# Performance work log

Measured on AMD Instinct MI355X. Metric: run time of the kernel, lower is better.

The kernel has to match this reference:

```python
import jax, jax.numpy as jnp
import numpy as np

D = 1024
N_HEADS = 16


def build_masks(H, W):
    # Row-major grid: token i -> (i // W, i % W). True = attend.
    idx = jnp.arange(H * W)
    r, c = idx // W, idx % W
    ri, rj = r[:, None], r[None, :]
    ci, cj = c[:, None], c[None, :]
    lr = (ri > rj) | ((ri == rj) & (ci >= cj))
    rl = (ri < rj) | ((ri == rj) & (ci <= cj))
    td = (ci > cj) | ((ci == cj) & (ri >= rj))
    bu = (ci < cj) | ((ci == cj) & (ri <= rj))
    return lr, rl, td, bu


def dir_attn(x, w_qkv, w_o, mask):
    # x: (B,T,D); w_qkv: (3D,D); w_o: (D,D); mask: (T,T) bool
    B, T, Dm = x.shape
    hd = Dm // N_HEADS
    qkv = (x @ w_qkv.T).reshape(B, T, 3, N_HEADS, hd)
    q = qkv[:, :, 0].transpose(0, 2, 1, 3)  # (B,H,T,hd)
    k = qkv[:, :, 1].transpose(0, 2, 1, 3)
    v = qkv[:, :, 2].transpose(0, 2, 1, 3)
    scores = jnp.einsum('bhqd,bhkd->bhqk', q, k) / np.sqrt(hd)
    scores = jnp.where(mask[None, None], scores, -jnp.inf)
    attn = jax.nn.softmax(scores, axis=-1)
    y = jnp.einsum('bhqk,bhkd->bhqd', attn, v)
    y = y.transpose(0, 2, 1, 3).reshape(B, T, Dm)
    return y @ w_o.T


def rmsnorm(x, w, eps=1e-6):
    norm = jax.lax.rsqrt(jnp.mean(jnp.square(x.astype(jnp.float32)), axis=-1, keepdims=True) + eps)
    return (x.astype(jnp.float32) * norm).astype(x.dtype) * w


def setup_inputs() -> dict:
    key = jax.random.key(0)
    ks = jax.random.split(key, 13)
    s = 0.02
    inp = {
        'x': jax.random.normal(ks[0], (4, 1024, D), dtype=jnp.float32),
        'w_qkv_lr': jax.random.normal(ks[1], (3 * D, D), dtype=jnp.float32) * s,
        'w_o_lr':   jax.random.normal(ks[2], (D, D), dtype=jnp.float32) * s,
        'w_qkv_rl': jax.random.normal(ks[3], (3 * D, D), dtype=jnp.float32) * s,
        'w_o_rl':   jax.random.normal(ks[4], (D, D), dtype=jnp.float32) * s,
        'w_qkv_td': jax.random.normal(ks[5], (3 * D, D), dtype=jnp.float32) * s,
        'w_o_td':   jax.random.normal(ks[6], (D, D), dtype=jnp.float32) * s,
        'w_qkv_bu': jax.random.normal(ks[7], (3 * D, D), dtype=jnp.float32) * s,
        'w_o_bu':   jax.random.normal(ks[8], (D, D), dtype=jnp.float32) * s,
        'w_gate':   jax.random.normal(ks[9], (4 * D, 4 * D), dtype=jnp.float32) * s,
        'b_gate':   jnp.zeros((4 * D,), dtype=jnp.float32),
        'w_out':    jax.random.normal(ks[10], (D, 4 * D), dtype=jnp.float32) * s,
        'norm_w':   jnp.ones((D,), dtype=jnp.float32),
        'grid_h': 32,
        'grid_w': 32,
    }
    return inp


def reference(x, w_qkv_lr, w_o_lr, w_qkv_rl, w_o_rl, w_qkv_td, w_o_td,
              w_qkv_bu, w_o_bu, w_gate, b_gate, w_out, norm_w, grid_h, grid_w):
    m_lr, m_rl, m_td, m_bu = build_masks(grid_h, grid_w)
    h_lr = dir_attn(x, w_qkv_lr, w_o_lr, m_lr)
    h_rl = dir_attn(x, w_qkv_rl, w_o_rl, m_rl)
    h_td = dir_attn(x, w_qkv_td, w_o_td, m_td)
    h_bu = dir_attn(x, w_qkv_bu, w_o_bu, m_bu)
    concat = jnp.concatenate([h_lr, h_rl, h_td, h_bu], axis=-1)  # (B,T,4D)
    gate = jax.nn.sigmoid(concat @ w_gate.T + b_gate)
    fused = (gate * concat) @ w_out.T
    return rmsnorm(fused + x, norm_w)
```

## Files before the change

### kernel.cpp

```cpp
#include <hip/hip_runtime.h>
#include <hip/hip_bf16.h>
#include <math.h>


typedef __bf16 bf16_t;
typedef __bf16 bf16x4 __attribute__((ext_vector_type(4)));
typedef __bf16 bf16x8 __attribute__((ext_vector_type(8)));
typedef float  f32x4  __attribute__((ext_vector_type(4)));

#define MFMA16(a, b, c) __builtin_amdgcn_mfma_f32_16x16x32_bf16((a), (b), (c), 0, 0, 0)

__device__ __forceinline__ void async16(const bf16_t* g, bf16_t* l) {
  __builtin_amdgcn_global_load_lds((const __attribute__((address_space(1))) void*)g,
                                   (__attribute__((address_space(3))) void*)l,
                                   16, 0, 0);
}

__device__ __forceinline__ float dpp_max16(float x) {
  float t;
  t = __builtin_bit_cast(float, __builtin_amdgcn_update_dpp(0, __builtin_bit_cast(int, x), 0xB1, 0xF, 0xF, true));
  x = fmaxf(x, t);
  t = __builtin_bit_cast(float, __builtin_amdgcn_update_dpp(0, __builtin_bit_cast(int, x), 0x4E, 0xF, 0xF, true));
  x = fmaxf(x, t);
  t = __builtin_bit_cast(float, __builtin_amdgcn_update_dpp(0, __builtin_bit_cast(int, x), 0x124, 0xF, 0xF, true));
  x = fmaxf(x, t);
  t = __builtin_bit_cast(float, __builtin_amdgcn_update_dpp(0, __builtin_bit_cast(int, x), 0x128, 0xF, 0xF, true));
  x = fmaxf(x, t);
  return x;
}
__device__ __forceinline__ float dpp_sum16(float x) {
  float t;
  t = __builtin_bit_cast(float, __builtin_amdgcn_update_dpp(0, __builtin_bit_cast(int, x), 0xB1, 0xF, 0xF, true));
  x += t;
  t = __builtin_bit_cast(float, __builtin_amdgcn_update_dpp(0, __builtin_bit_cast(int, x), 0x4E, 0xF, 0xF, true));
  x += t;
  t = __builtin_bit_cast(float, __builtin_amdgcn_update_dpp(0, __builtin_bit_cast(int, x), 0x124, 0xF, 0xF, true));
  x += t;
  t = __builtin_bit_cast(float, __builtin_amdgcn_update_dpp(0, __builtin_bit_cast(int, x), 0x128, 0xF, 0xF, true));
  x += t;
  return x;
}

struct Ptr4 { const bf16_t* p[4]; };

__device__ __forceinline__ int perm_t(int p, int dir) {
  int q = (dir & 1) ? (1023 - p) : p;
  if (dir >= 2) q = ((q & 31) << 5) | (q >> 5);
  return q;
}

struct CvtDesc {
  const float* src[9];
  bf16_t* dst[9];
  int n8[9];
};

__device__ __forceinline__ void cvt8(const float* in, bf16_t* out, int i) {
  const float4 a = ((const float4*)in)[i * 2];
  const float4 b = ((const float4*)in)[i * 2 + 1];
  bf16x8 o;
  o[0] = (bf16_t)a.x; o[1] = (bf16_t)a.y; o[2] = (bf16_t)a.z; o[3] = (bf16_t)a.w;
  o[4] = (bf16_t)b.x; o[5] = (bf16_t)b.y; o[6] = (bf16_t)b.z; o[7] = (bf16_t)b.w;
  ((bf16x8*)out)[i] = o;
}

__global__ __launch_bounds__(256) void cvt9_k(CvtDesc d) {
  const int seg = blockIdx.y;
  const int i = blockIdx.x * 256 + threadIdx.x;
  if (i >= d.n8[seg]) return;
  cvt8(d.src[seg], d.dst[seg], i);
}

template <int MODE>
__global__ __launch_bounds__(512, 2) void gemm_bt2(
    const bf16_t* __restrict__ A, long sAz, int lda,
    Ptr4 B4, int ldb,
    void* __restrict__ Cv, long sCz, int ldc, int K, int koff,
    const float* __restrict__ bias,
    const bf16_t* __restrict__ gin,
    bf16_t* __restrict__ vtp, long sVz, int dirbase) {
  constexpr int BM = 256, BN = 256, BK = 64;
  (void)BM; (void)BN;
  __shared__ __align__(16) char smem[131072];

  const int z = blockIdx.z;
  const bf16_t* Ap = A + (long)z * sAz;
  const bf16_t* Bp = B4.p[z];
  const int tid = threadIdx.x;
  const int lane = tid & 63;
  const int wave = tid >> 6;
  const int l15 = lane & 15, qd = lane >> 4;
  const int wm = wave >> 2, wn = wave & 3;
  const int bm = blockIdx.y * 256, bn = blockIdx.x * 256;
  const int kz = (MODE == 3) ? z * koff : 0;
  const int NT = K / BK;

  const int row0 = tid >> 3;
  const int blkp = ((tid & 7) ^ (row0 & 7)) * 8;
  const bf16_t* gA = Ap + (long)(bm + row0) * lda + blkp + kz;
  const bf16_t* gB = Bp + (long)(bn + row0) * ldb + blkp + kz;
  char* const sm = (char*)smem;
  const int ldsT = tid * 16;

  const int xorv = (l15 & 7) << 4;
  const int aBase = (wm * 128 + l15) * 128;
  const int bBase = 32768 + (wn * 64 + l15) * 128;
  const int colk0 = (qd * 16) ^ xorv;
  const int colk1 = (64 + qd * 16) ^ xorv;

  f32x4 acc[8][4];
#pragma unroll
  for (int i = 0; i < 8; i++)
#pragma unroll
    for (int j = 0; j < 4; j++) acc[i][j] = (f32x4){0.f, 0.f, 0.f, 0.f};

#pragma unroll
  for (int u = 0; u < 4; u++)
    async16(gA + (long)(u * 64) * lda, (bf16_t*)(sm + u * 8192 + ldsT));
#pragma unroll
  for (int u = 0; u < 4; u++)
    async16(gB + (long)(u * 64) * ldb, (bf16_t*)(sm + 32768 + u * 8192 + ldsT));
  asm volatile("s_waitcnt vmcnt(0)" ::: "memory");
  __builtin_amdgcn_s_barrier();

  for (int kt = 0; kt < NT; ++kt) {
    const int c = kt & 1;
    const char* sa = sm + c * 65536;
    const int nb = (c ^ 1) * 65536;
    const long ko = (long)(kt + 1) * BK;
    bf16x8 bF[4][2];
#pragma unroll
    for (int p = 0; p < 4; ++p) {
      if (p == 0) {
#pragma unroll
        for (int n = 0; n < 4; ++n) {
          bF[n][0] = *(const bf16x8*)(sa + bBase + n * 2048 + colk0);
          bF[n][1] = *(const bf16x8*)(sa + bBase + n * 2048 + colk1);
        }
      }
      bf16x8 aF[2][2];
#pragma unroll
      for (int mm = 0; mm < 2; ++mm) {
        aF[mm][0] = *(const bf16x8*)(sa + aBase + (p * 2 + mm) * 2048 + colk0);
        aF[mm][1] = *(const bf16x8*)(sa + aBase + (p * 2 + mm) * 2048 + colk1);
      }
      if (kt + 1 < NT) {
        if (p == 0) {
#pragma unroll
          for (int u = 0; u < 4; u++)
            async16(gA + (long)(u * 64) * lda + ko,
                    (bf16_t*)(sm + nb + u * 8192 + ldsT));
        } else if (p == 1) {
#pragma unroll
          for (int u = 0; u < 4; u++)
            async16(gB + (long)(u * 64) * ldb + ko,
                    (bf16_t*)(sm + nb + 32768 + u * 8192 + ldsT));
        }
      }
      __builtin_amdgcn_s_barrier();
      asm volatile("s_waitcnt lgkmcnt(0)" ::: "memory");
      __builtin_amdgcn_s_setprio(1);
#pragma unroll
      for (int kh = 0; kh < 2; ++kh)
#pragma unroll
        for (int mm = 0; mm < 2; ++mm)
#pragma unroll
          for (int n = 0; n < 4; ++n)
            acc[p * 2 + mm][n] =
                MFMA16(aF[mm][kh], bF[n][kh], acc[p * 2 + mm][n]);
      __builtin_amdgcn_s_setprio(0);
      __builtin_amdgcn_s_barrier();
    }
    if (kt + 1 < NT) {
      asm volatile("s_waitcnt vmcnt(0)" ::: "memory");
      __builtin_amdgcn_s_barrier();
    }
  }

  if constexpr (MODE == 4) {
    const int dir = dirbase + z;
    if (bn < 2048) {
      bf16_t* qkz = (bf16_t*)Cv + (long)z * sCz;
      float* sC = (float*)smem;
#pragma unroll
      for (int p = 0; p < 4; ++p) {
        if (p) __syncthreads();
        if (wm == (p >> 1)) {
#pragma unroll
          for (int mm = 0; mm < 4; ++mm) {
            const int m = (p & 1) * 4 + mm;
#pragma unroll
            for (int n = 0; n < 4; ++n)
#pragma unroll
              for (int r = 0; r < 4; ++r)
                sC[(mm * 16 + qd * 4 + r) * 260 + wn * 64 + n * 16 + l15] =
                    acc[m][n][r];
          }
        }
        __syncthreads();
#pragma unroll
        for (int i = 0; i < 8; ++i) {
          const int idx = i * 512 + tid;
          const int rl = idx >> 6, c4 = (idx & 63) * 4;
          const float4 v4 = *(const float4*)&sC[rl * 260 + c4];
          const int grow = bm + p * 64 + rl;
          const int prow = (grow & ~1023) | perm_t(grow & 1023, dir);
          bf16x4 o;
          o[0] = (bf16_t)v4.x; o[1] = (bf16_t)v4.y;
          o[2] = (bf16_t)v4.z; o[3] = (bf16_t)v4.w;
          *(bf16x4*)(qkz + (long)prow * ldc + bn + c4) = o;
        }
      }
    } else {
      bf16_t* vz = vtp + (long)z * sVz;
      float* sCt = (float*)smem;
#pragma unroll
      for (int p = 0; p < 4; ++p) {
        if (p) __syncthreads();
        if (wm == (p >> 1)) {
#pragma unroll
          for (int mm = 0; mm < 4; ++mm) {
            const int m = (p & 1) * 4 + mm;
#pragma unroll
            for (int n = 0; n < 4; ++n)
#pragma unroll
              for (int r = 0; r < 4; ++r)
                sCt[(wn * 64 + n * 16 + l15) * 68 + mm * 16 + qd * 4 + r] =
                    acc[m][n][r];
          }
        }
        __syncthreads();
#pragma unroll
        for (int i = 0; i < 8; ++i) {
          const int idx = i * 512 + tid;
          const int col = idx >> 4, tq = idx & 15;
          const float4 v4 = *(const float4*)&sCt[col * 68 + tq * 4];
          const int t0 = (bm & 1023) + p * 64 + tq * 4;
          const int bb = bm >> 10;
          const int ch = bn + col - 2048;
          bf16_t* vrow =
              vz + (((long)bb * 16 + (ch >> 6)) * 64 + (ch & 63)) * 1024;
          if (dir == 0) {
            bf16x4 o;
            o[0] = (bf16_t)v4.x; o[1] = (bf16_t)v4.y;
            o[2] = (bf16_t)v4.z; o[3] = (bf16_t)v4.w;
            *(bf16x4*)(vrow + t0) = o;
          } else if (dir == 1) {
            bf16x4 o;
            o[0] = (bf16_t)v4.w; o[1] = (bf16_t)v4.z;
            o[2] = (bf16_t)v4.y; o[3] = (bf16_t)v4.x;
            *(bf16x4*)(vrow + (1020 - t0)) = o;
          } else {
            vrow[perm_t(t0 + 0, dir)] = (bf16_t)v4.x;
            vrow[perm_t(t0 + 1, dir)] = (bf16_t)v4.y;
            vrow[perm_t(t0 + 2, dir)] = (bf16_t)v4.z;
            vrow[perm_t(t0 + 3, dir)] = (bf16_t)v4.w;
          }
        }
      }
    }
  } else {
    float* sC = (float*)smem;
#pragma unroll
    for (int p = 0; p < 4; ++p) {
      if (p) __syncthreads();
      if (wm == (p >> 1)) {
#pragma unroll
        for (int mm = 0; mm < 4; ++mm) {
          const int m = (p & 1) * 4 + mm;
#pragma unroll
          for (int n = 0; n < 4; ++n)
#pragma unroll
            for (int r = 0; r < 4; ++r)
              sC[(mm * 16 + qd * 4 + r) * 260 + wn * 64 + n * 16 + l15] =
                  acc[m][n][r];
        }
      }
      __syncthreads();
#pragma unroll
      for (int i = 0; i < 8; ++i) {
        const int idx = i * 512 + tid;
        const int rl = idx >> 6, c4 = (idx & 63) * 4;
        const float4 v4 = *(const float4*)&sC[rl * 260 + c4];
        const int grow = bm + p * 64 + rl;
        const int gcol = bn + c4;
        const long goff = (long)grow * ldc + gcol;
        if constexpr (MODE == 0) {
          bf16x4 o;
          o[0] = (bf16_t)v4.x; o[1] = (bf16_t)v4.y;
          o[2] = (bf16_t)v4.z; o[3] = (bf16_t)v4.w;
          *(bf16x4*)((bf16_t*)Cv + (long)z * sCz + goff) = o;
        } else if constexpr (MODE == 1) {
          const float4 bb = *(const float4*)&bias[gcol];
          const bf16x4 gv = *(const bf16x4*)&gin[goff];
          bf16x4 o;
          o[0] = (bf16_t)((float)gv[0] / (1.f + __expf(-(v4.x + bb.x))));
          o[1] = (bf16_t)((float)gv[1] / (1.f + __expf(-(v4.y + bb.y))));
          o[2] = (bf16_t)((float)gv[2] / (1.f + __expf(-(v4.z + bb.z))));
          o[3] = (bf16_t)((float)gv[3] / (1.f + __expf(-(v4.w + bb.w))));
          *(bf16x4*)((bf16_t*)Cv + goff) = o;
        } else {
          *(float4*)((float*)Cv + (long)z * sCz + goff) = v4;
        }
      }
    }
  }
}

template <int MODE>
__global__ __launch_bounds__(256) void gemm_bt(
    const bf16_t* __restrict__ A, long sAz, int lda,
    Ptr4 B4, int ldb,
    void* __restrict__ Cv, long sCz, int ldc, int K, int koff,
    const float* __restrict__ bias,
    const bf16_t* __restrict__ gin,
    bf16_t* __restrict__ vtp, long sVz, int dirbase) {
  constexpr int BM = 128, BN = 128, BK = 32;
  __shared__ __align__(16) char smem[18432];
  bf16_t* sA = (bf16_t*)smem;
  bf16_t* sB = (bf16_t*)(smem + BM * BK * 2);
  float* sC = (float*)smem;

  const int z = blockIdx.z;
  const bf16_t* Ap = A + (long)z * sAz;
  const bf16_t* Bp = B4.p[z];
  const int tid = threadIdx.x;
  const int wave = tid >> 6, lane = tid & 63;
  const int lane15 = lane & 15, quad = lane >> 4;
  const int bm = blockIdx.y * BM, bn = blockIdx.x * BN;
  const int wm = (wave >> 1) * 64, wn = (wave & 1) * 64;

  f32x4 acc[4][4];
#pragma unroll
  for (int i = 0; i < 4; i++)
#pragma unroll
    for (int j = 0; j < 4; j++) acc[i][j] = (f32x4){0.f, 0.f, 0.f, 0.f};

  const int srow = wave * 16 + (lane >> 2);
  const int skoff = (lane & 3) * 8;
  const int kz = (MODE == 3) ? z * koff : 0;
  const bf16_t* ga = Ap + (long)(bm + srow) * lda + skoff + kz;
  const bf16_t* gb = Bp + (long)(bn + srow) * ldb + skoff + kz;
  bf16_t* la = &sA[srow * BK + skoff];
  bf16_t* lb = &sB[srow * BK + skoff];

  for (int k0 = 0; k0 < K; k0 += BK) {
    __syncthreads();
    async16(ga + k0, la);
    async16(ga + k0 + (long)64 * lda, la + 64 * BK);
    async16(gb + k0, lb);
    async16(gb + k0 + (long)64 * ldb, lb + 64 * BK);
    __syncthreads();

    bf16x8 af[4], bfv[4];
#pragma unroll
    for (int i = 0; i < 4; i++)
      af[i] = *(const bf16x8*)&sA[(wm + i * 16 + lane15) * BK + quad * 8];
#pragma unroll
    for (int j = 0; j < 4; j++)
      bfv[j] = *(const bf16x8*)&sB[(wn + j * 16 + lane15) * BK + quad * 8];
#pragma unroll
    for (int i = 0; i < 4; i++)
#pragma unroll
      for (int j = 0; j < 4; j++)
        acc[i][j] = MFMA16(af[i], bfv[j], acc[i][j]);
  }

  __syncthreads();

  if constexpr (MODE == 4) {
    const int dir = dirbase + z;
    if (bn < 2048) {
      bf16_t* qkz = (bf16_t*)Cv + (long)z * sCz;
#pragma unroll
      for (int p = 0; p < 4; p++) {
        if (p) __syncthreads();
        const int sr = (wm >> 2) + quad * 4;
#pragma unroll
        for (int r = 0; r < 4; r++)
#pragma unroll
          for (int j = 0; j < 4; j++)
            sC[(sr + r) * 144 + wn + j * 16 + lane15] = acc[p][j][r];
        __syncthreads();
#pragma unroll
        for (int c = 0; c < 4; c++) {
          const int idx = c * 256 + tid;
          const int srr = idx >> 5, chunk = idx & 31;
          const float4 v4 = *(const float4*)&sC[srr * 144 + chunk * 4];
          const int grow = bm + p * 16 + (srr & 15) + (srr >> 4) * 64;
          const int prow = (grow & ~1023) | perm_t(grow & 1023, dir);
          bf16x4 o;
          o[0] = (bf16_t)v4.x; o[1] = (bf16_t)v4.y;
          o[2] = (bf16_t)v4.z; o[3] = (bf16_t)v4.w;
          *(bf16x4*)(qkz + (long)prow * 2048 + bn + chunk * 4) = o;
        }
      }
    } else {
      bf16_t* vz = vtp + (long)z * sVz;
      float* sCt = sC;
#pragma unroll
      for (int p = 0; p < 2; p++)
#pragma unroll
        for (int q = 0; q < 2; q++) {
          if (p || q) __syncthreads();
          if ((wave & 1) == q) {
#pragma unroll
            for (int ii = 0; ii < 2; ii++) {
              const int i = 2 * p + ii;
              const int srb = (wm >> 1) + ii * 16 + quad * 4;
#pragma unroll
              for (int r = 0; r < 4; r++)
#pragma unroll
                for (int j = 0; j < 4; j++)
                  sCt[(j * 16 + lane15) * 68 + srb + r] = acc[i][j][r];
            }
          }
          __syncthreads();
#pragma unroll
          for (int c = 0; c < 4; c++) {
            const int idx = c * 256 + tid;
            const int col = idx >> 4, tq = idx & 15;
            const int srr0 = (tq & 7) * 4 + (tq >> 3) * 32;
            const float4 v4 = *(const float4*)&sCt[col * 68 + srr0];
            const int t0 = (bm & 1023) + p * 32 + (srr0 & 31) + (srr0 >> 5) * 64;
            const int bb = bm >> 10;
            const int ch = bn + 64 * q + col - 2048;
            bf16_t* vrow =
                vz + (((long)bb * 16 + (ch >> 6)) * 64 + (ch & 63)) * 1024;
            if (dir == 0) {
              bf16x4 o;
              o[0] = (bf16_t)v4.x; o[1] = (bf16_t)v4.y;
              o[2] = (bf16_t)v4.z; o[3] = (bf16_t)v4.w;
              *(bf16x4*)(vrow + t0) = o;
            } else if (dir == 1) {
              bf16x4 o;
              o[0] = (bf16_t)v4.w; o[1] = (bf16_t)v4.z;
              o[2] = (bf16_t)v4.y; o[3] = (bf16_t)v4.x;
              *(bf16x4*)(vrow + (1020 - t0)) = o;
            } else {
              vrow[perm_t(t0 + 0, dir)] = (bf16_t)v4.x;
              vrow[perm_t(t0 + 1, dir)] = (bf16_t)v4.y;
              vrow[perm_t(t0 + 2, dir)] = (bf16_t)v4.z;
              vrow[perm_t(t0 + 3, dir)] = (bf16_t)v4.w;
            }
          }
        }
    }
  } else {
#pragma unroll
    for (int p = 0; p < 4; p++) {
      if (p) __syncthreads();
      const int sr = (wm >> 2) + quad * 4;
#pragma unroll
      for (int r = 0; r < 4; r++)
#pragma unroll
        for (int j = 0; j < 4; j++)
          sC[(sr + r) * 144 + wn + j * 16 + lane15] = acc[p][j][r];
      __syncthreads();
#pragma unroll
      for (int c = 0; c < 4; c++) {
        const int idx = c * 256 + tid;
        const int srr = idx >> 5, chunk = idx & 31;
        const float4 v4 = *(const float4*)&sC[srr * 144 + chunk * 4];
        const int grow = bm + p * 16 + (srr & 15) + (srr >> 4) * 64;
        const int gcol = bn + chunk * 4;
        const long goff = (long)grow * ldc + gcol;
        if constexpr (MODE == 0) {
          bf16x4 o;
          o[0] = (bf16_t)v4.x; o[1] = (bf16_t)v4.y;
          o[2] = (bf16_t)v4.z; o[3] = (bf16_t)v4.w;
          *(bf16x4*)((bf16_t*)Cv + (long)z * sCz + goff) = o;
        } else if constexpr (MODE == 1) {
          const float4 bb = *(const float4*)&bias[gcol];
          const bf16x4 gv = *(const bf16x4*)&gin[goff];
          bf16x4 o;
          o[0] = (bf16_t)((float)gv[0] / (1.f + __expf(-(v4.x + bb.x))));
          o[1] = (bf16_t)((float)gv[1] / (1.f + __expf(-(v4.y + bb.y))));
          o[2] = (bf16_t)((float)gv[2] / (1.f + __expf(-(v4.z + bb.z))));
          o[3] = (bf16_t)((float)gv[3] / (1.f + __expf(-(v4.w + bb.w))));
          *(bf16x4*)((bf16_t*)Cv + goff) = o;
        } else {
          *(float4*)((float*)Cv + (long)z * sCz + goff) = v4;
        }
      }
    }
  }
}

__global__ __launch_bounds__(256, 3) void attn_k(
    const bf16_t* __restrict__ qk, long sQz,
    const bf16_t* __restrict__ vt, long sVz,
    bf16_t* __restrict__ y, long sYz, int dir0) {
  const int zi = blockIdx.y >> 6;
  const int bh = blockIdx.y & 63;
  const int dir = dir0 + zi;
  const int b = bh >> 4, h = bh & 15;
  const int qt = (int)(gridDim.x - 1 - blockIdx.x);
  const int tid = threadIdx.x;
  const int wave = tid >> 6, lane = tid & 63;
  const int lane15 = lane & 15, quad = lane >> 4;
  const int hoff = h * 64;
  const bf16_t* base = qk + (long)zi * sQz + (long)b * 1024 * 2048;
  const bf16_t* vth = vt + (long)zi * sVz + ((long)b * 16 + h) * 64 * 1024;
  bf16_t* yd = y + (long)zi * sYz;

  __shared__ __align__(16) bf16_t sK[64 * 72];
  __shared__ __align__(16) bf16_t sVt[64 * 72];
  __shared__ __align__(16) bf16_t sP[4][32 * 72];

  bf16x8 qa[2][2];
#pragma unroll
  for (int g = 0; g < 2; g++) {
    const int row = qt * 128 + wave * 32 + g * 16 + lane15;
    qa[g][0] = *(const bf16x8*)(base + (long)row * 2048 + hoff + quad * 8);
    qa[g][1] = *(const bf16x8*)(base + (long)row * 2048 + hoff + 32 + quad * 8);
  }

  const float FNEG = -1e30f;
  float mrow[2][4], lrow[2][4];
  f32x4 o[2][4];
#pragma unroll
  for (int g = 0; g < 2; g++)
#pragma unroll
    for (int r = 0; r < 4; r++) { mrow[g][r] = FNEG; lrow[g][r] = 0.f; }
#pragma unroll
  for (int g = 0; g < 2; g++)
#pragma unroll
    for (int d4 = 0; d4 < 4; d4++) o[g][d4] = (f32x4){0.f, 0.f, 0.f, 0.f};

  const int krow = tid >> 3, kd = (tid & 7) * 8;
  const int vd = tid >> 2, pc = (tid & 3) * 8;
  const bf16_t* kb_g = base + 1024 + hoff;

  bf16x8 kA = *(const bf16x8*)(kb_g + (long)krow * 2048 + kd);
  bf16x8 kB = *(const bf16x8*)(kb_g + (long)(32 + krow) * 2048 + kd);
  bf16x8 vA = *(const bf16x8*)(vth + (long)vd * 1024 + pc);
  bf16x8 vB = *(const bf16x8*)(vth + (long)vd * 1024 + 32 + pc);

  const int ktiles = 2 * qt + 2;
  for (int kt = 0; kt < ktiles; kt++) {
    __syncthreads();
    *(bf16x8*)&sK[krow * 72 + kd] = kA;
    *(bf16x8*)&sK[(krow + 32) * 72 + kd] = kB;
    *(bf16x8*)&sVt[vd * 72 + pc] = vA;
    *(bf16x8*)&sVt[vd * 72 + 32 + pc] = vB;
    __syncthreads();
    if (kt + 1 < ktiles) {
      const int nb = (kt + 1) * 64;
      kA = *(const bf16x8*)(kb_g + (long)(nb + krow) * 2048 + kd);
      kB = *(const bf16x8*)(kb_g + (long)(nb + 32 + krow) * 2048 + kd);
      vA = *(const bf16x8*)(vth + (long)vd * 1024 + nb + pc);
      vB = *(const bf16x8*)(vth + (long)vd * 1024 + nb + 32 + pc);
    }
    const int kbase = kt * 64;

    bf16x8 kb[4][2];
#pragma unroll
    for (int ns = 0; ns < 4; ns++) {
      kb[ns][0] = *(const bf16x8*)&sK[(ns * 16 + lane15) * 72 + quad * 8];
      kb[ns][1] = *(const bf16x8*)&sK[(ns * 16 + lane15) * 72 + 32 + quad * 8];
    }
    f32x4 s[2][4];
#pragma unroll
    for (int g = 0; g < 2; g++)
#pragma unroll
      for (int ns = 0; ns < 4; ns++) {
        f32x4 t = (f32x4){0.f, 0.f, 0.f, 0.f};
        t = MFMA16(qa[g][0], kb[ns][0], t);
        t = MFMA16(qa[g][1], kb[ns][1], t);
        s[g][ns] = t;
      }
#pragma unroll
    for (int g = 0; g < 2; g++) {
      const int qc = qt * 128 + wave * 32 + g * 16 + quad * 4;
#pragma unroll
      for (int ns = 0; ns < 4; ns++) {
        const int kp = kbase + ns * 16 + lane15;
#pragma unroll
        for (int r = 0; r < 4; r++) {
          const float v = s[g][ns][r] * 0.125f;
          s[g][ns][r] = (kp <= qc + r) ? v : FNEG;
        }
      }
    }
#pragma unroll
    for (int g = 0; g < 2; g++) {
      float alpha[4];
#pragma unroll
      for (int r = 0; r < 4; r++) {
        float tm = fmaxf(fmaxf(s[g][0][r], s[g][1][r]),
                         fmaxf(s[g][2][r], s[g][3][r]));
        tm = dpp_max16(tm);
        const float mn = fmaxf(mrow[g][r], tm);
        alpha[r] = __expf(mrow[g][r] - mn);
        mrow[g][r] = mn;
      }
#pragma unroll
      for (int ns = 0; ns < 4; ns++)
#pragma unroll
        for (int r = 0; r < 4; r++)
          s[g][ns][r] = __expf(s[g][ns][r] - mrow[g][r]);
#pragma unroll
      for (int r = 0; r < 4; r++) {
        float ts = (s[g][0][r] + s[g][1][r]) + (s[g][2][r] + s[g][3][r]);
        ts = dpp_sum16(ts);
        lrow[g][r] = lrow[g][r] * alpha[r] + ts;
      }
#pragma unroll
      for (int d4 = 0; d4 < 4; d4++)
#pragma unroll
        for (int r = 0; r < 4; r++) o[g][d4][r] *= alpha[r];
#pragma unroll
      for (int ns = 0; ns < 4; ns++)
#pragma unroll
        for (int r = 0; r < 4; r++)
          sP[wave][(g * 16 + quad * 4 + r) * 72 + ns * 16 + lane15] =
              (bf16_t)s[g][ns][r];
    }
    bf16x8 vb[4][2];
#pragma unroll
    for (int d4 = 0; d4 < 4; d4++) {
      vb[d4][0] = *(const bf16x8*)&sVt[(d4 * 16 + lane15) * 72 + quad * 8];
      vb[d4][1] = *(const bf16x8*)&sVt[(d4 * 16 + lane15) * 72 + 32 + quad * 8];
    }
#pragma unroll
    for (int g = 0; g < 2; g++) {
      const bf16x8 pa0 = *(const bf16x8*)&sP[wave][(g * 16 + lane15) * 72 + quad * 8];
      const bf16x8 pa1 = *(const bf16x8*)&sP[wave][(g * 16 + lane15) * 72 + 32 + quad * 8];
#pragma unroll
      for (int d4 = 0; d4 < 4; d4++) {
        o[g][d4] = MFMA16(pa0, vb[d4][0], o[g][d4]);
        o[g][d4] = MFMA16(pa1, vb[d4][1], o[g][d4]);
      }
    }
  }

#pragma unroll
  for (int g = 0; g < 2; g++)
#pragma unroll
    for (int r = 0; r < 4; r++) {
      const float rinv = 1.f / fmaxf(lrow[g][r], 1e-20f);
#pragma unroll
      for (int d4 = 0; d4 < 4; d4++)
        sP[wave][(g * 16 + quad * 4 + r) * 72 + d4 * 16 + lane15] =
            (bf16_t)(o[g][d4][r] * rinv);
    }
#pragma unroll
  for (int g = 0; g < 2; g++) {
    const bf16x8 o0 = *(const bf16x8*)&sP[wave][(g * 16 + lane15) * 72 + quad * 16];
    const bf16x8 o1 = *(const bf16x8*)&sP[wave][(g * 16 + lane15) * 72 + quad * 16 + 8];
    const int tok = perm_t(qt * 128 + wave * 32 + g * 16 + lane15, dir);
    bf16_t* yr = yd + ((long)b * 1024 + tok) * 1024 + hoff + quad * 16;
    *(bf16x8*)yr = o0;
    *(bf16x8*)(yr + 8) = o1;
  }
}

__global__ __launch_bounds__(256) void rmsnorm_k(const float* __restrict__ p0,
                                                 const float* __restrict__ p1,
                                                 const float* __restrict__ p2,
                                                 const float* __restrict__ p3,
                                                 const float* __restrict__ x,
                                                 const float* __restrict__ w,
                                                 float* __restrict__ out) {
  const int row = blockIdx.x, tid = threadIdx.x;
  const long off = (long)row * 1024;
  const float4 a = ((const float4*)(p0 + off))[tid];
  const float4 bq = ((const float4*)(p1 + off))[tid];
  const float4 c = ((const float4*)(x + off))[tid];
  float4 v;
  v.x = a.x + bq.x + c.x;
  v.y = a.y + bq.y + c.y;
  v.z = a.z + bq.z + c.z;
  v.w = a.w + bq.w + c.w;
  if (p2) {
    const float4 d = ((const float4*)(p2 + off))[tid];
    const float4 e = ((const float4*)(p3 + off))[tid];
    v.x += d.x + e.x;
    v.y += d.y + e.y;
    v.z += d.z + e.z;
    v.w += d.w + e.w;
  }
  float ss = v.x * v.x + v.y * v.y + v.z * v.z + v.w * v.w;
#pragma unroll
  for (int o2 = 32; o2 >= 1; o2 >>= 1) ss += __shfl_xor(ss, o2);
  __shared__ float wsum[4];
  if ((tid & 63) == 0) wsum[tid >> 6] = ss;
  __syncthreads();
  const float tot = wsum[0] + wsum[1] + wsum[2] + wsum[3];
  const float norm = rsqrtf(tot * (1.f / 1024.f) + 1e-6f);
  const float4 wv = ((const float4*)w)[tid];
  v.x = v.x * norm * wv.x;
  v.y = v.y * norm * wv.y;
  v.z = v.z * norm * wv.z;
  v.w = v.w * norm * wv.w;
  ((float4*)(out + off))[tid] = v;
}

extern "C" void kernel_launch(void* const* d_in, const int* in_sizes, int n_in,
                              void* d_out, int out_size, void* d_ws, size_t ws_size,
                              hipStream_t stream) {
  (void)in_sizes; (void)n_in; (void)out_size;
  const float* xf = (const float*)d_in[0];
  const float* wqkv_f[4] = {(const float*)d_in[1], (const float*)d_in[3],
                            (const float*)d_in[5], (const float*)d_in[7]};
  const float* wo_f[4] = {(const float*)d_in[2], (const float*)d_in[4],
                          (const float*)d_in[6], (const float*)d_in[8]};
  const float* wgate_f = (const float*)d_in[9];
  const float* bgate_f = (const float*)d_in[10];
  const float* wout_f = (const float*)d_in[11];
  const float* normw_f = (const float*)d_in[12];

  const long MB = 1l << 20;
  char* ws = (char*)d_ws;
  const dim3 blk(256);
  const dim3 blk2(512);
  const bool batched = ws_size >= (size_t)(168 * MB);
  const long sQK = 4096l * 2048;
  const long sVT = 4096l * 1024;
  const long sY  = 4096l * 1024;

  if (batched) {
    bf16_t* x_c    = (bf16_t*)(ws);
    bf16_t* wq_c   = (bf16_t*)(ws + 8 * MB);
    bf16_t* wo_c   = (bf16_t*)(ws + 32 * MB);
    bf16_t* qk     = (bf16_t*)(ws + 40 * MB);
    bf16_t* vt     = (bf16_t*)(ws + 104 * MB);
    bf16_t* y      = (bf16_t*)(ws + 136 * MB);
    bf16_t* concat = (bf16_t*)(ws + 40 * MB);
    bf16_t* wg_c   = (bf16_t*)(ws + 72 * MB);
    bf16_t* wout_c = (bf16_t*)(ws);
    float*  part4  = (float*)(ws + 40 * MB);
    bf16_t* gated  = y;

    {
      CvtDesc cd;
      cd.src[0] = xf; cd.dst[0] = x_c; cd.n8[0] = 4194304 / 8;
      for (int d = 0; d < 4; d++) {
        cd.src[1 + d] = wqkv_f[d];
        cd.dst[1 + d] = wq_c + (long)d * 3145728;
        cd.n8[1 + d] = 3145728 / 8;
        cd.src[5 + d] = wo_f[d];
        cd.dst[5 + d] = wo_c + (long)d * 1048576;
        cd.n8[5 + d] = 1048576 / 8;
      }
      cvt9_k<<<dim3(2048, 9), blk, 0, stream>>>(cd);
    }
    {
      Ptr4 bq{{wq_c, wq_c + 3145728, wq_c + 2l * 3145728, wq_c + 3l * 3145728}};
      gemm_bt2<4><<<dim3(12, 16, 4), blk2, 0, stream>>>(
          x_c, 0, 1024, bq, 1024, qk, sQK, 2048, 1024, 0, nullptr, nullptr,
          vt, sVT, 0);
    }
    attn_k<<<dim3(8, 256), blk, 0, stream>>>(qk, sQK, vt, sVT, y, sY, 0);
    {
      CvtDesc cd;
      for (int s = 0; s < 9; s++) cd.n8[s] = 0;
      cd.src[0] = wgate_f; cd.dst[0] = wg_c; cd.n8[0] = 16777216 / 8;
      cd.src[1] = wout_f; cd.dst[1] = wout_c; cd.n8[1] = 4194304 / 8;
      cvt9_k<<<dim3(8192, 2), blk, 0, stream>>>(cd);
    }
    {
      Ptr4 b4{{wo_c, wo_c + 1048576, wo_c + 2097152, wo_c + 3145728}};
      gemm_bt2<0><<<dim3(4, 16, 4), blk2, 0, stream>>>(
          y, sY, 1024, b4, 1024, concat, 1024, 4096, 1024, 0, nullptr, nullptr,
          nullptr, 0, 0);
    }
    {
      Ptr4 b4{{wg_c, wg_c, wg_c, wg_c}};
      gemm_bt2<1><<<dim3(16, 16, 1), blk2, 0, stream>>>(
          concat, 0, 4096, b4, 4096, gated, 0, 4096, 4096, 0, bgate_f, concat,
          nullptr, 0, 0);
    }
    {
      Ptr4 b4{{wout_c, wout_c, wout_c, wout_c}};
      gemm_bt2<3><<<dim3(4, 16, 4), blk2, 0, stream>>>(
          gated, 0, 4096, b4, 4096, part4, (long)4096 * 1024, 1024, 1024, 1024,
          nullptr, nullptr, nullptr, 0, 0);
    }
    rmsnorm_k<<<dim3(4096), blk, 0, stream>>>(
        part4, part4 + (long)4096 * 1024, part4 + 2l * 4096 * 1024,
        part4 + 3l * 4096 * 1024, xf, normw_f, (float*)d_out);
  } else {
    bf16_t* x_c    = (bf16_t*)(ws);
    bf16_t* wq_c   = (bf16_t*)(ws + 8 * MB);
    bf16_t* qk_d   = (bf16_t*)(ws + 32 * MB);
    bf16_t* vt_d   = (bf16_t*)(ws + 48 * MB);
    bf16_t* wo_c   = (bf16_t*)(ws + 56 * MB);
    bf16_t* y      = (bf16_t*)(ws + 64 * MB);
    bf16_t* concat = (bf16_t*)(ws);
    bf16_t* wg_c   = (bf16_t*)(ws + 32 * MB);
    bf16_t* wout_c = (bf16_t*)(ws);
    float*  part   = (float*)(ws + 8 * MB);
    bf16_t* gated  = y;

    {
      CvtDesc cd;
      cd.src[0] = xf; cd.dst[0] = x_c; cd.n8[0] = 4194304 / 8;
      for (int d = 0; d < 4; d++) {
        cd.src[1 + d] = wqkv_f[d];
        cd.dst[1 + d] = wq_c + (long)d * 3145728;
        cd.n8[1 + d] = 3145728 / 8;
        cd.src[5 + d] = wo_f[d];
        cd.dst[5 + d] = wo_c + (long)d * 1048576;
        cd.n8[5 + d] = 1048576 / 8;
      }
      cvt9_k<<<dim3(2048, 9), blk, 0, stream>>>(cd);
    }
    for (int d = 0; d < 4; d++) {
      const bf16_t* wq_d = wq_c + (long)d * 3145728;
      Ptr4 bq{{wq_d, wq_d, wq_d, wq_d}};
      gemm_bt<4><<<dim3(24, 32, 1), blk, 0, stream>>>(
          x_c, 0, 1024, bq, 1024, qk_d, 0, 2048, 1024, 0, nullptr, nullptr,
          vt_d, 0, d);
      attn_k<<<dim3(8, 64), blk, 0, stream>>>(qk_d, 0, vt_d, 0,
                                              y + (long)d * sY, 0, d);
    }
    {
      Ptr4 b4{{wo_c, wo_c + 1048576, wo_c + 2097152, wo_c + 3145728}};
      gemm_bt<0><<<dim3(8, 32, 4), blk, 0, stream>>>(
          y, sY, 1024, b4, 1024, concat, 1024, 4096, 1024, 0, nullptr, nullptr,
          nullptr, 0, 0);
    }
    {
      CvtDesc cd;
      for (int s = 0; s < 9; s++) cd.n8[s] = 0;
      cd.src[0] = wgate_f; cd.dst[0] = wg_c; cd.n8[0] = 16777216 / 8;
      cvt9_k<<<dim3(8192, 1), blk, 0, stream>>>(cd);
    }
    {
      Ptr4 b4{{wg_c, wg_c, wg_c, wg_c}};
      gemm_bt<1><<<dim3(32, 32, 1), blk, 0, stream>>>(
          concat, 0, 4096, b4, 4096, gated, 0, 4096, 4096, 0, bgate_f, concat,
          nullptr, 0, 0);
    }
    {
      CvtDesc cd;
      for (int s = 0; s < 9; s++) cd.n8[s] = 0;
      cd.src[0] = wout_f; cd.dst[0] = wout_c; cd.n8[0] = 4194304 / 8;
      cvt9_k<<<dim3(2048, 1), blk, 0, stream>>>(cd);
    }
    {
      Ptr4 b4{{wout_c, wout_c, wout_c, wout_c}};
      gemm_bt<3><<<dim3(8, 32, 2), blk, 0, stream>>>(
          gated, 0, 4096, b4, 4096, part, (long)4096 * 1024, 1024, 2048, 2048,
          nullptr, nullptr, nullptr, 0, 0);
    }
    rmsnorm_k<<<dim3(4096), blk, 0, stream>>>(part, part + (long)4096 * 1024,
                                              nullptr, nullptr,
                                              xf, normw_f, (float*)d_out);
  }
}
```

Measured before the change: 697.2 us.

## Pair causal query tiles per attention block and fold softmax scale into K

Each attention block now handles two query tiles, a long one and a short one (7-bx and bx), so causal work is balanced across blocks. Block indices are remapped with a swizzle, likely to improve L2 locality. The 1/sqrt(hd) scale moves into the K epilogue of the QKV GEMM, so the attention loop no longer multiplies every score. Masking runs only on diagonal tiles, and the O/l rescale is skipped when no row max changes. The GEMM mainloop drops one barrier per k-step by merging the vmcnt wait into the last sub-step. Launch bounds are raised to 4 waves per SIMD, which may increase register pressure or cause spills.

```diff
diff --git a/kernel.cpp b/kernel.cpp
--- a/kernel.cpp
+++ b/kernel.cpp
@@ -169,10 +169,8 @@
             acc[p * 2 + mm][n] =
                 MFMA16(aF[mm][kh], bF[n][kh], acc[p * 2 + mm][n]);
       __builtin_amdgcn_s_setprio(0);
-      __builtin_amdgcn_s_barrier();
-    }
-    if (kt + 1 < NT) {
-      asm volatile("s_waitcnt vmcnt(0)" ::: "memory");
+      if (p == 3 && kt + 1 < NT)
+        asm volatile("s_waitcnt vmcnt(0)" ::: "memory");
       __builtin_amdgcn_s_barrier();
     }
   }
@@ -181,6 +179,7 @@
     const int dir = dirbase + z;
     if (bn < 2048) {
       bf16_t* qkz = (bf16_t*)Cv + (long)z * sCz;
+      const float ksc = (bn >= 1024) ? 0.125f : 1.0f;
       float* sC = (float*)smem;
 #pragma unroll
       for (int p = 0; p < 4; ++p) {
@@ -206,8 +205,8 @@
           const int grow = bm + p * 64 + rl;
           const int prow = (grow & ~1023) | perm_t(grow & 1023, dir);
           bf16x4 o;
-          o[0] = (bf16_t)v4.x; o[1] = (bf16_t)v4.y;
-          o[2] = (bf16_t)v4.z; o[3] = (bf16_t)v4.w;
+          o[0] = (bf16_t)(v4.x * ksc); o[1] = (bf16_t)(v4.y * ksc);
+          o[2] = (bf16_t)(v4.z * ksc); o[3] = (bf16_t)(v4.w * ksc);
           *(bf16x4*)(qkz + (long)prow * ldc + bn + c4) = o;
         }
       }
@@ -372,6 +371,7 @@
     const int dir = dirbase + z;
     if (bn < 2048) {
       bf16_t* qkz = (bf16_t*)Cv + (long)z * sCz;
+      const float ksc = (bn >= 1024) ? 0.125f : 1.0f;
 #pragma unroll
       for (int p = 0; p < 4; p++) {
         if (p) __syncthreads();
@@ -390,8 +390,8 @@
           const int grow = bm + p * 16 + (srr & 15) + (srr >> 4) * 64;
           const int prow = (grow & ~1023) | perm_t(grow & 1023, dir);
           bf16x4 o;
-          o[0] = (bf16_t)v4.x; o[1] = (bf16_t)v4.y;
-          o[2] = (bf16_t)v4.z; o[3] = (bf16_t)v4.w;
+          o[0] = (bf16_t)(v4.x * ksc); o[1] = (bf16_t)(v4.y * ksc);
+          o[2] = (bf16_t)(v4.z * ksc); o[3] = (bf16_t)(v4.w * ksc);
           *(bf16x4*)(qkz + (long)prow * 2048 + bn + chunk * 4) = o;
         }
       }
@@ -487,15 +487,18 @@
   }
 }
 
-__global__ __launch_bounds__(256, 3) void attn_k(
+__global__ __launch_bounds__(256, 4) void attn_k(
     const bf16_t* __restrict__ qk, long sQz,
     const bf16_t* __restrict__ vt, long sVz,
     bf16_t* __restrict__ y, long sYz, int dir0) {
-  const int zi = blockIdx.y >> 6;
-  const int bh = blockIdx.y & 63;
+  const int p0 = blockIdx.y * 4 + blockIdx.x;
+  const int chunk = gridDim.y >> 1;
+  const int lg = (p0 & 7) * chunk + (p0 >> 3);
+  const int bx = lg & 3, by = lg >> 2;
+  const int zi = by >> 6;
+  const int bh = by & 63;
   const int dir = dir0 + zi;
   const int b = bh >> 4, h = bh & 15;
-  const int qt = (int)(gridDim.x - 1 - blockIdx.x);
   const int tid = threadIdx.x;
   const int wave = tid >> 6, lane = tid & 63;
   const int lane15 = lane & 15, quad = lane >> 4;
@@ -508,151 +511,173 @@
   __shared__ __align__(16) bf16_t sVt[64 * 72];
   __shared__ __align__(16) bf16_t sP[4][32 * 72];
 
-  bf16x8 qa[2][2];
-#pragma unroll
-  for (int g = 0; g < 2; g++) {
-    const int row = qt * 128 + wave * 32 + g * 16 + lane15;
-    qa[g][0] = *(const bf16x8*)(base + (long)row * 2048 + hoff + quad * 8);
-    qa[g][1] = *(const bf16x8*)(base + (long)row * 2048 + hoff + 32 + quad * 8);
-  }
-
-  const float FNEG = -1e30f;
-  float mrow[2][4], lrow[2][4];
-  f32x4 o[2][4];
-#pragma unroll
-  for (int g = 0; g < 2; g++)
-#pragma unroll
-    for (int r = 0; r < 4; r++) { mrow[g][r] = FNEG; lrow[g][r] = 0.f; }
-#pragma unroll
-  for (int g = 0; g < 2; g++)
-#pragma unroll
-    for (int d4 = 0; d4 < 4; d4++) o[g][d4] = (f32x4){0.f, 0.f, 0.f, 0.f};
-
   const int krow = tid >> 3, kd = (tid & 7) * 8;
   const int vd = tid >> 2, pc = (tid & 3) * 8;
   const bf16_t* kb_g = base + 1024 + hoff;
-
-  bf16x8 kA = *(const bf16x8*)(kb_g + (long)krow * 2048 + kd);
-  bf16x8 kB = *(const bf16x8*)(kb_g + (long)(32 + krow) * 2048 + kd);
-  bf16x8 vA = *(const bf16x8*)(vth + (long)vd * 1024 + pc);
-  bf16x8 vB = *(const bf16x8*)(vth + (long)vd * 1024 + 32 + pc);
-
-  const int ktiles = 2 * qt + 2;
-  for (int kt = 0; kt < ktiles; kt++) {
-    __syncthreads();
-    *(bf16x8*)&sK[krow * 72 + kd] = kA;
-    *(bf16x8*)&sK[(krow + 32) * 72 + kd] = kB;
-    *(bf16x8*)&sVt[vd * 72 + pc] = vA;
-    *(bf16x8*)&sVt[vd * 72 + 32 + pc] = vB;
-    __syncthreads();
-    if (kt + 1 < ktiles) {
-      const int nb = (kt + 1) * 64;
-      kA = *(const bf16x8*)(kb_g + (long)(nb + krow) * 2048 + kd);
-      kB = *(const bf16x8*)(kb_g + (long)(nb + 32 + krow) * 2048 + kd);
-      vA = *(const bf16x8*)(vth + (long)vd * 1024 + nb + pc);
-      vB = *(const bf16x8*)(vth + (long)vd * 1024 + nb + 32 + pc);
-    }
-    const int kbase = kt * 64;
-
-    bf16x8 kb[4][2];
-#pragma unroll
-    for (int ns = 0; ns < 4; ns++) {
-      kb[ns][0] = *(const bf16x8*)&sK[(ns * 16 + lane15) * 72 + quad * 8];
-      kb[ns][1] = *(const bf16x8*)&sK[(ns * 16 + lane15) * 72 + 32 + quad * 8];
-    }
-    f32x4 s[2][4];
+  const float FNEG = -1e30f;
+
+  for (int pass = 0; pass < 2; ++pass) {
+    const int qt = pass ? bx : 7 - bx;
+
+    bf16x8 qa[2][2];
+#pragma unroll
+    for (int g = 0; g < 2; g++) {
+      const int row = qt * 128 + wave * 32 + g * 16 + lane15;
+      qa[g][0] = *(const bf16x8*)(base + (long)row * 2048 + hoff + quad * 8);
+      qa[g][1] = *(const bf16x8*)(base + (long)row * 2048 + hoff + 32 + quad * 8);
+    }
+
+    float mrow[2][4], lrow[2][4];
+    f32x4 o[2][4];
 #pragma unroll
     for (int g = 0; g < 2; g++)
 #pragma unroll
+      for (int r = 0; r < 4; r++) { mrow[g][r] = FNEG; lrow[g][r] = 0.f; }
+#pragma unroll
+    for (int g = 0; g < 2; g++)
+#pragma unroll
+      for (int d4 = 0; d4 < 4; d4++) o[g][d4] = (f32x4){0.f, 0.f, 0.f, 0.f};
+
+    bf16x8 kA = *(const bf16x8*)(kb_g + (long)krow * 2048 + kd);
+    bf16x8 kB = *(const bf16x8*)(kb_g + (long)(32 + krow) * 2048 + kd);
+    bf16x8 vA = *(const bf16x8*)(vth + (long)vd * 1024 + pc);
+    bf16x8 vB = *(const bf16x8*)(vth + (long)vd * 1024 + 32 + pc);
+
+    const int qlo = qt * 128 + wave * 32;
+    const int ktiles = 2 * qt + 2;
+    for (int kt = 0; kt < ktiles; kt++) {
+      __syncthreads();
+      *(bf16x8*)&sK[krow * 72 + kd] = kA;
+      *(bf16x8*)&sK[(krow + 32) * 72 + kd] = kB;
+      *(bf16x8*)&sVt[vd * 72 + pc] = vA;
+      *(bf16x8*)&sVt[vd * 72 + 32 + pc] = vB;
+      __syncthreads();
+      if (kt + 1 < ktiles) {
+        const int nb = (kt + 1) * 64;
+        kA = *(const bf16x8*)(kb_g + (long)(nb + krow) * 2048 + kd);
+        kB = *(const bf16x8*)(kb_g + (long)(nb + 32 + krow) * 2048 + kd);
+        vA = *(const bf16x8*)(vth + (long)vd * 1024 + nb + pc);
+        vB = *(const bf16x8*)(vth + (long)vd * 1024 + nb + 32 + pc);
+      }
+      const int kbase = kt * 64;
+
+      bf16x8 kb[4][2];
+#pragma unroll
       for (int ns = 0; ns < 4; ns++) {
-        f32x4 t = (f32x4){0.f, 0.f, 0.f, 0.f};
-        t = MFMA16(qa[g][0], kb[ns][0], t);
-        t = MFMA16(qa[g][1], kb[ns][1], t);
-        s[g][ns] = t;
+        kb[ns][0] = *(const bf16x8*)&sK[(ns * 16 + lane15) * 72 + quad * 8];
+        kb[ns][1] = *(const bf16x8*)&sK[(ns * 16 + lane15) * 72 + 32 + quad * 8];
+      }
+      f32x4 s[2][4];
+#pragma unroll
+      for (int g = 0; g < 2; g++)
+#pragma unroll
+        for (int ns = 0; ns < 4; ns++) {
+          f32x4 t = (f32x4){0.f, 0.f, 0.f, 0.f};
+          t = MFMA16(qa[g][0], kb[ns][0], t);
+          t = MFMA16(qa[g][1], kb[ns][1], t);
+          s[g][ns] = t;
+        }
+      if (kbase + 63 > qlo) {
+#pragma unroll
+        for (int g = 0; g < 2; g++) {
+          const int qc = qlo + g * 16 + quad * 4;
+#pragma unroll
+          for (int ns = 0; ns < 4; ns++) {
+            const int kp = kbase + ns * 16 + lane15;
+#pragma unroll
+            for (int r = 0; r < 4; r++)
+              if (kp > qc + r) s[g][ns][r] = FNEG;
+          }
+        }
+      }
+      float tm[2][4];
+#pragma unroll
+      for (int g = 0; g < 2; g++)
+#pragma unroll
+        for (int r = 0; r < 4; r++) {
+          float t = fmaxf(fmaxf(s[g][0][r], s[g][1][r]),
+                          fmaxf(s[g][2][r], s[g][3][r]));
+          tm[g][r] = dpp_max16(t);
+        }
+      bool up = false;
+#pragma unroll
+      for (int g = 0; g < 2; g++)
+#pragma unroll
+        for (int r = 0; r < 4; r++) up = up || (tm[g][r] > mrow[g][r]);
+      if (__any(up)) {
+#pragma unroll
+        for (int g = 0; g < 2; g++) {
+          float alpha[4];
+#pragma unroll
+          for (int r = 0; r < 4; r++) {
+            const float mn = fmaxf(mrow[g][r], tm[g][r]);
+            alpha[r] = __expf(mrow[g][r] - mn);
+            mrow[g][r] = mn;
+          }
+#pragma unroll
+          for (int r = 0; r < 4; r++) lrow[g][r] *= alpha[r];
+#pragma unroll
+          for (int d4 = 0; d4 < 4; d4++)
+#pragma unroll
+            for (int r = 0; r < 4; r++) o[g][d4][r] *= alpha[r];
+        }
+      }
+#pragma unroll
+      for (int g = 0; g < 2; g++) {
+#pragma unroll
+        for (int ns = 0; ns < 4; ns++)
+#pragma unroll
+          for (int r = 0; r < 4; r++)
+            s[g][ns][r] = __expf(s[g][ns][r] - mrow[g][r]);
+#pragma unroll
+        for (int r = 0; r < 4; r++) {
+          float ts = (s[g][0][r] + s[g][1][r]) + (s[g][2][r] + s[g][3][r]);
+          lrow[g][r] += dpp_sum16(ts);
+        }
+#pragma unroll
+        for (int ns = 0; ns < 4; ns++)
+#pragma unroll
+          for (int r = 0; r < 4; r++)
+            sP[wave][(g * 16 + quad * 4 + r) * 72 + ns * 16 + lane15] =
+                (bf16_t)s[g][ns][r];
+      }
+      bf16x8 vb[4][2];
+#pragma unroll
+      for (int d4 = 0; d4 < 4; d4++) {
+        vb[d4][0] = *(const bf16x8*)&sVt[(d4 * 16 + lane15) * 72 + quad * 8];
+        vb[d4][1] = *(const bf16x8*)&sVt[(d4 * 16 + lane15) * 72 + 32 + quad * 8];
+      }
+#pragma unroll
+      for (int g = 0; g < 2; g++) {
+        const bf16x8 pa0 = *(const bf16x8*)&sP[wave][(g * 16 + lane15) * 72 + quad * 8];
+        const bf16x8 pa1 = *(const bf16x8*)&sP[wave][(g * 16 + lane15) * 72 + 32 + quad * 8];
+#pragma unroll
+        for (int d4 = 0; d4 < 4; d4++) {
+          o[g][d4] = MFMA16(pa0, vb[d4][0], o[g][d4]);
+          o[g][d4] = MFMA16(pa1, vb[d4][1], o[g][d4]);
+        }
+      }
+    }
+
+#pragma unroll
+    for (int g = 0; g < 2; g++)
+#pragma unroll
+      for (int r = 0; r < 4; r++) {
+        const float rinv = 1.f / fmaxf(lrow[g][r], 1e-20f);
+#pragma unroll
+        for (int d4 = 0; d4 < 4; d4++)
+          sP[wave][(g * 16 + quad * 4 + r) * 72 + d4 * 16 + lane15] =
+              (bf16_t)(o[g][d4][r] * rinv);
       }
 #pragma unroll
     for (int g = 0; g < 2; g++) {
-      const int qc = qt * 128 + wave * 32 + g * 16 + quad * 4;
-#pragma unroll
-      for (int ns = 0; ns < 4; ns++) {
-        const int kp = kbase + ns * 16 + lane15;
-#pragma unroll
-        for (int r = 0; r < 4; r++) {
-          const float v = s[g][ns][r] * 0.125f;
-          s[g][ns][r] = (kp <= qc + r) ? v : FNEG;
-        }
-      }
-    }
-#pragma unroll
-    for (int g = 0; g < 2; g++) {
-      float alpha[4];
-#pragma unroll
-      for (int r = 0; r < 4; r++) {
-        float tm = fmaxf(fmaxf(s[g][0][r], s[g][1][r]),
-                         fmaxf(s[g][2][r], s[g][3][r]));
-        tm = dpp_max16(tm);
-        const float mn = fmaxf(mrow[g][r], tm);
-        alpha[r] = __expf(mrow[g][r] - mn);
-        mrow[g][r] = mn;
-      }
-#pragma unroll
-      for (int ns = 0; ns < 4; ns++)
-#pragma unroll
-        for (int r = 0; r < 4; r++)
-          s[g][ns][r] = __expf(s[g][ns][r] - mrow[g][r]);
-#pragma unroll
-      for (int r = 0; r < 4; r++) {
-        float ts = (s[g][0][r] + s[g][1][r]) + (s[g][2][r] + s[g][3][r]);
-        ts = dpp_sum16(ts);
-        lrow[g][r] = lrow[g][r] * alpha[r] + ts;
-      }
-#pragma unroll
-      for (int d4 = 0; d4 < 4; d4++)
-#pragma unroll
-        for (int r = 0; r < 4; r++) o[g][d4][r] *= alpha[r];
-#pragma unroll
-      for (int ns = 0; ns < 4; ns++)
-#pragma unroll
-        for (int r = 0; r < 4; r++)
-          sP[wave][(g * 16 + quad * 4 + r) * 72 + ns * 16 + lane15] =
-              (bf16_t)s[g][ns][r];
-    }
-    bf16x8 vb[4][2];
-#pragma unroll
-    for (int d4 = 0; d4 < 4; d4++) {
-      vb[d4][0] = *(const bf16x8*)&sVt[(d4 * 16 + lane15) * 72 + quad * 8];
-      vb[d4][1] = *(const bf16x8*)&sVt[(d4 * 16 + lane15) * 72 + 32 + quad * 8];
-    }
-#pragma unroll
-    for (int g = 0; g < 2; g++) {
-      const bf16x8 pa0 = *(const bf16x8*)&sP[wave][(g * 16 + lane15) * 72 + quad * 8];
-      const bf16x8 pa1 = *(const bf16x8*)&sP[wave][(g * 16 + lane15) * 72 + 32 + quad * 8];
-#pragma unroll
-      for (int d4 = 0; d4 < 4; d4++) {
-        o[g][d4] = MFMA16(pa0, vb[d4][0], o[g][d4]);
-        o[g][d4] = MFMA16(pa1, vb[d4][1], o[g][d4]);
-      }
-    }
-  }
-
-#pragma unroll
-  for (int g = 0; g < 2; g++)
-#pragma unroll
-    for (int r = 0; r < 4; r++) {
-      const float rinv = 1.f / fmaxf(lrow[g][r], 1e-20f);
-#pragma unroll
-      for (int d4 = 0; d4 < 4; d4++)
-        sP[wave][(g * 16 + quad * 4 + r) * 72 + d4 * 16 + lane15] =
-            (bf16_t)(o[g][d4][r] * rinv);
-    }
-#pragma unroll
-  for (int g = 0; g < 2; g++) {
-    const bf16x8 o0 = *(const bf16x8*)&sP[wave][(g * 16 + lane15) * 72 + quad * 16];
-    const bf16x8 o1 = *(const bf16x8*)&sP[wave][(g * 16 + lane15) * 72 + quad * 16 + 8];
-    const int tok = perm_t(qt * 128 + wave * 32 + g * 16 + lane15, dir);
-    bf16_t* yr = yd + ((long)b * 1024 + tok) * 1024 + hoff + quad * 16;
-    *(bf16x8*)yr = o0;
-    *(bf16x8*)(yr + 8) = o1;
+      const bf16x8 o0 = *(const bf16x8*)&sP[wave][(g * 16 + lane15) * 72 + quad * 16];
+      const bf16x8 o1 = *(const bf16x8*)&sP[wave][(g * 16 + lane15) * 72 + quad * 16 + 8];
+      const int tok = perm_t(qt * 128 + wave * 32 + g * 16 + lane15, dir);
+      bf16_t* yr = yd + ((long)b * 1024 + tok) * 1024 + hoff + quad * 16;
+      *(bf16x8*)yr = o0;
+      *(bf16x8*)(yr + 8) = o1;
+    }
   }
 }
 
@@ -752,7 +777,7 @@
           x_c, 0, 1024, bq, 1024, qk, sQK, 2048, 1024, 0, nullptr, nullptr,
           vt, sVT, 0);
     }
-    attn_k<<<dim3(8, 256), blk, 0, stream>>>(qk, sQK, vt, sVT, y, sY, 0);
+    attn_k<<<dim3(4, 256), blk, 0, stream>>>(qk, sQK, vt, sVT, y, sY, 0);
     {
       CvtDesc cd;
       for (int s = 0; s < 9; s++) cd.n8[s] = 0;
@@ -813,7 +838,7 @@
       gemm_bt<4><<<dim3(24, 32, 1), blk, 0, stream>>>(
           x_c, 0, 1024, bq, 1024, qk_d, 0, 2048, 1024, 0, nullptr, nullptr,
           vt_d, 0, d);
-      attn_k<<<dim3(8, 64), blk, 0, stream>>>(qk_d, 0, vt_d, 0,
+      attn_k<<<dim3(4, 64), blk, 0, stream>>>(qk_d, 0, vt_d, 0,
                                               y + (long)d * sY, 0, d);
     }
     {
```

New measurement: 724.6 us. 1.04x slower.
